# Kernel tuning notes

Measured on AMD Instinct MI355X. Metric: run time of the kernel, lower is better.

The kernel has to match this reference:

```python
import jax, jax.numpy as jnp
import numpy as np

# config constants (match init_kwargs)
C = 1024
NH = 16
HS = C // NH
CHUNK = 64          # attn_chunk_size
TOPK = 32           # attn_topk
WINDOW = 4096       # kv_cache_window_size
MIN_KV = 16384      # min_kv_cache_size
MAX_KV = 32768      # max_kv_cache_size
SHORT = 4096        # short_sequence_criteria
CT = 65536          # incoming kv-cache length


def setup_inputs() -> dict:
    key = jax.random.key(0)
    ks = jax.random.split(key, 7)
    s = 1.0 / np.sqrt(C)
    return {
        "x": jax.random.normal(ks[0], (C,), jnp.float32),
        "k_cache": jax.random.normal(ks[1], (1, CT, C), jnp.float32),
        "v_cache": jax.random.normal(ks[2], (1, CT, C), jnp.float32),
        "Wr": jax.random.normal(ks[3], (C, C), jnp.float32) * s,
        "Wk": jax.random.normal(ks[4], (C, C), jnp.float32) * s,
        "Wv": jax.random.normal(ks[5], (C, C), jnp.float32) * s,
        "Wo": jax.random.normal(ks[6], (C, C), jnp.float32) * s,
    }


def _split_heads(t):  # (1, T, C) -> (1, NH, T, HS)
    return t.reshape(1, t.shape[1], NH, HS).transpose(0, 2, 1, 3)


def _update_kv_cache(q, k_cache, v_cache):
    # q: (1,1,C); caches: (1,CT,C). CT > MIN_KV so compression runs.
    past = CT - WINDOW
    kp = _split_heads(k_cache[:, :past])          # (1,NH,past,HS)
    vp = _split_heads(v_cache[:, :past])
    qh = _split_heads(q)                          # (1,NH,1,HS)
    scores = jnp.einsum("bhqd,bhkd->bhqk", qh, kp) / np.sqrt(HS)
    w = jax.nn.softmax(scores, axis=-1)           # (1,NH,1,past)
    vote = w.sum(axis=-2)                         # (1,NH,past)
    keep = MIN_KV - WINDOW                        # per-head tokens kept
    _, idx = jax.lax.top_k(vote, keep)            # (1,NH,keep), descending vote order
    kpc = jnp.take_along_axis(kp, idx[..., None], axis=2)  # (1,NH,keep,HS)
    vpc = jnp.take_along_axis(vp, idx[..., None], axis=2)
    kpc = kpc.transpose(0, 2, 1, 3).reshape(1, keep, C)
    vpc = vpc.transpose(0, 2, 1, 3).reshape(1, keep, C)
    k_new = jnp.concatenate([kpc, k_cache[:, past:]], axis=1)  # (1, MIN_KV, C)
    v_new = jnp.concatenate([vpc, v_cache[:, past:]], axis=1)
    return k_new, v_new


def reference(x, k_cache, v_cache, Wr, Wk, Wv, Wo):
    x2 = x[None, None, :]                         # (1,1,C)
    q = x2 @ Wr.T
    k = x2 @ Wk.T
    v = x2 @ Wv.T

    # CT > MAX_KV -> compress cache (eviction via attention vote per head)
    k_cache, v_cache = _update_kv_cache(q, k_cache, v_cache)
    CT2 = k_cache.shape[1]                        # MIN_KV = 16384 > SHORT -> sparse path

    num_chunks = CT2 // CHUNK
    kc = k_cache.reshape(1, num_chunks, CHUNK, C)
    vc = v_cache.reshape(1, num_chunks, CHUNK, C)
    chunk_key = kc.mean(axis=2)                   # (1,num_chunks,C)
    chunk_score = jnp.einsum("bqc,bkc->bqk", q, chunk_key)
    _, tidx = jax.lax.top_k(chunk_score[0, 0], TOPK)  # (TOPK,)
    topk_k = kc[:, tidx].reshape(1, TOPK * CHUNK, C)
    topk_v = vc[:, tidx].reshape(1, TOPK * CHUNK, C)

    k_comb = jnp.concatenate([topk_k, k], axis=1)  # (1, TOPK*CHUNK+1, C)
    v_comb = jnp.concatenate([topk_v, v], axis=1)

    qh = _split_heads(q)                          # (1,NH,1,HS)
    kh = _split_heads(k_comb)
    vh = _split_heads(v_comb)
    attn = jax.nn.softmax(
        jnp.einsum("bhqd,bhkd->bhqk", qh, kh) / np.sqrt(HS), axis=-1)
    y = jnp.einsum("bhqk,bhkd->bhqd", attn, vh)   # (1,NH,1,HS)
    y = y.transpose(0, 2, 1, 3).reshape(C)
    y = y @ Wo.T
    return y
```

## Files before the change

### kernel.cpp

```cpp
#include <hip/hip_runtime.h>
#include <stdint.h>

#define C      1024
#define NH     16
#define HS     64
#define CT     65536
#define PAST   61440
#define KEEP   12288
#define NCOMP  192
#define NSEL   32
#define NB     8192
#define NBLK   256
#define FLAGW  8

typedef unsigned long long ull;

#define LD_A(p)   __hip_atomic_load((p), __ATOMIC_RELAXED, __HIP_MEMORY_SCOPE_AGENT)
#define ST_A(p,v) __hip_atomic_store((p), (v), __ATOMIC_RELAXED, __HIP_MEMORY_SCOPE_AGENT)

__device__ __forceinline__ unsigned int desc_key(float f) {
    unsigned int b = __float_as_uint(f);
    return (b >> 31) ? b : (~b & 0x7FFFFFFFu);
}
__device__ __forceinline__ float u_to_f(unsigned int u) {
    unsigned int b = (u & 0x80000000u) ? u : (0x7FFFFFFFu - u);
    return __uint_as_float(b);
}
__device__ __forceinline__ int bin_of(float s, float hi, float scale) {
    int b = (int)((hi - s) * scale);
    return b < 0 ? 0 : (b > NB - 1 ? NB - 1 : b);
}
__device__ __forceinline__ void load_params(const unsigned* umin, const unsigned* umax,
                                            int h, float* hi, float* sc) {
    float h2 = u_to_f(umin[h]);
    float lo = u_to_f(umax[h]);
    float r = h2 - lo;
    *hi = h2;
    *sc = (r > 0.f) ? (float)(NB - 1) / r : 0.f;
}

__device__ __forceinline__ void arrive(unsigned* flag, unsigned ph) {
    __syncthreads();
    if (threadIdx.x == 0) {
        asm volatile("s_waitcnt vmcnt(0)" ::: "memory");
        ST_A(&flag[blockIdx.x * FLAGW], ph);
    }
}
__device__ __forceinline__ void wait_head(unsigned* flag, unsigned ph, int h) {
    if (threadIdx.x < 16)
        while (LD_A(&flag[(h * 16 + threadIdx.x) * FLAGW]) < ph)
            __builtin_amdgcn_s_sleep(2);
    __syncthreads();
}
__device__ __forceinline__ void wait_all(unsigned* flag, unsigned ph) {
    if (threadIdx.x < 256)
        while (LD_A(&flag[threadIdx.x * FLAGW]) < ph)
            __builtin_amdgcn_s_sleep(2);
    __syncthreads();
}

__global__ void k_proj(const float* __restrict__ x, const float* __restrict__ Wr,
                       const float* __restrict__ Wk, const float* __restrict__ Wv,
                       float* __restrict__ q, float* __restrict__ kn, float* __restrict__ vn,
                       unsigned* __restrict__ hc, unsigned* __restrict__ umin,
                       unsigned* __restrict__ umax, ull* __restrict__ cs_fix,
                       unsigned* __restrict__ flag) {
    int gid = blockIdx.x * 256 + threadIdx.x;
    for (int i = gid; i < 2 * NH * NB; i += 196608) hc[i] = 0;
    if (blockIdx.x >= 512 && blockIdx.x < 520)
        flag[(blockIdx.x - 512) * 256 + threadIdx.x] = 0u;
    if (blockIdx.x == 700) {
        if (threadIdx.x < 16) umin[threadIdx.x] = 0xFFFFFFFFu;
        else if (threadIdx.x < 32) umax[threadIdx.x - 16] = 0u;
    }
    if (blockIdx.x == 701 && threadIdx.x < 256) cs_fix[threadIdx.x] = 0ull;

    int w = blockIdx.x * (blockDim.x >> 6) + (threadIdx.x >> 6);
    int lane = threadIdx.x & 63;
    int mat = w >> 10, row = w & 1023;
    const float* W = (mat == 0) ? Wr : (mat == 1) ? Wk : Wv;
    const float4* Wrow = (const float4*)(W + (size_t)row * C);
    const float4* x4 = (const float4*)x;
    float acc = 0.f;
#pragma unroll
    for (int i = 0; i < 4; ++i) {
        float4 a = Wrow[i * 64 + lane];
        float4 b = x4[i * 64 + lane];
        acc += a.x * b.x + a.y * b.y + a.z * b.z + a.w * b.w;
    }
#pragma unroll
    for (int off = 32; off; off >>= 1) acc += __shfl_xor(acc, off);
    if (lane == 0) { (mat == 0 ? q : (mat == 1 ? kn : vn))[row] = acc; }
}

__global__ __launch_bounds__(1024, 2) void k_mega(
        const float* __restrict__ kc, const float* __restrict__ vc,
        unsigned* __restrict__ umin, unsigned* __restrict__ umax,
        unsigned* __restrict__ hist, unsigned* __restrict__ cnt,
        ull* __restrict__ G, ull* __restrict__ stokv,
        ull* __restrict__ cs_fix, float* __restrict__ part,
        const float* __restrict__ q, const float* __restrict__ kn,
        const float* __restrict__ vn, const float* __restrict__ Wo,
        float* __restrict__ yg, float* __restrict__ out,
        float* __restrict__ s_win, unsigned* __restrict__ flag) {
    const int bid = blockIdx.x, tid = threadIdx.x;
    const int lane = tid & 63, wave = tid >> 6;
    const int h = bid >> 4, seg = bid & 15;
    __shared__ __align__(16) char smem[50688];
    __shared__ unsigned shT, shN;
    __shared__ unsigned wsum[16];
    __shared__ float smn[16], smx[16];

    float* s_lds = (float*)smem;
    unsigned* lh = (unsigned*)(smem + 16384);

    {
        const int t_base = seg * 4096;
        const int g = lane >> 4;
        float4 qv = ((const float4*)q)[h * 16 + (lane & 15)];
        float mn = 3.4e38f, mx = -3.4e38f;
        for (int ib = 0; ib < 64; ib += 4) {
            float4 av[4];
#pragma unroll
            for (int u = 0; u < 4; ++u) {
                int lt = wave * 256 + (ib + u) * 4 + g;
                av[u] = ((const float4*)(kc + (size_t)(t_base + lt) * C + h * HS))[lane & 15];
            }
#pragma unroll
            for (int u = 0; u < 4; ++u) {
                float d = av[u].x * qv.x + av[u].y * qv.y + av[u].z * qv.z + av[u].w * qv.w;
#pragma unroll
                for (int off = 8; off; off >>= 1) d += __shfl_xor(d, off);
                int lt = wave * 256 + (ib + u) * 4 + g;
                if ((lane & 15) == 0) s_lds[lt] = d;
                mn = fminf(mn, d);
                mx = fmaxf(mx, d);
            }
        }
        __syncthreads();
        if (seg < 15) {
#pragma unroll
            for (int off = 32; off; off >>= 1) {
                mn = fminf(mn, __shfl_xor(mn, off));
                mx = fmaxf(mx, __shfl_xor(mx, off));
            }
            if (lane == 0) { smn[wave] = mn; smx[wave] = mx; }
            __syncthreads();
            if (tid == 0) {
                float bmn = smn[0], bmx = smx[0];
                for (int w2 = 1; w2 < 16; ++w2) {
                    bmn = fminf(bmn, smn[w2]);
                    bmx = fmaxf(bmx, smx[w2]);
                }
                atomicMin(&umin[h], desc_key(bmx));
                atomicMax(&umax[h], desc_key(bmn));
            }
        } else {
            for (int i = tid; i < 4096; i += 1024)
                ST_A(&s_win[h * 4096 + i], s_lds[i]);
            int c = tid >> 4;
            long long f = 0;
#pragma unroll
            for (int j = 0; j < 4; ++j)
                f += llrintf(s_lds[c * 64 + (tid & 15) * 4 + j] * 16777216.f);
#pragma unroll
            for (int off = 8; off; off >>= 1) f += __shfl_xor(f, off);
            if ((tid & 15) == 0) atomicAdd(&cs_fix[NCOMP + c], (ull)f);
        }
    }
    arrive(flag, 1); wait_head(flag, 1, h);

    float hi, sc; load_params(umin, umax, h, &hi, &sc);

    {
        for (int i = tid; i < NB; i += 1024) lh[i] = 0;
        __syncthreads();
        if (seg < 15) {
            for (int i = tid; i < 4096; i += 1024)
                atomicAdd(&lh[bin_of(s_lds[i], hi, sc)], 1u);
            __syncthreads();
            unsigned* gh = hist + h * NB;
            for (int i = tid; i < NB; i += 1024) {
                unsigned c = lh[i];
                if (c) atomicAdd(&gh[i], c);
            }
        }
    }
    arrive(flag, 2); wait_head(flag, 2, h);

    {
        const unsigned* gh = hist + h * NB;
        unsigned c8[8]; unsigned loc = 0; int b0 = tid * 8;
#pragma unroll
        for (int k = 0; k < 8; ++k) { c8[k] = gh[b0 + k]; loc += c8[k]; }
        unsigned run = loc;
#pragma unroll
        for (int off = 1; off < 64; off <<= 1) {
            unsigned n = __shfl_up(run, off);
            if (lane >= off) run += n;
        }
        if (lane == 63) wsum[wave] = run;
        __syncthreads();
        if (wave == 0 && lane < 16) {
            unsigned v = wsum[lane];
#pragma unroll
            for (int off = 1; off < 16; off <<= 1) {
                unsigned n = __shfl_up(v, off);
                if (lane >= off) v += n;
            }
            wsum[lane] = v;
        }
        __syncthreads();
        unsigned r = run - loc + (wave ? wsum[wave - 1] : 0u);
#pragma unroll
        for (int k = 0; k < 8; ++k) {
            unsigned c = c8[k];
            lh[b0 + k] = r;
            unsigned inc = r + c;
            if (r < KEEP && inc >= KEEP) { shT = (unsigned)(b0 + k); shN = inc; }
            r = inc;
        }
    }
    __syncthreads();
    const unsigned T = shT, ncand = shN;

    if (seg < 15) {
        unsigned* ch = cnt + h * NB;
        ull* Gh = G + (size_t)h * 65536;
        const int t_base = seg * 4096;
        for (int i = tid; i < 4096; i += 1024) {
            float v = s_lds[i];
            int b = bin_of(v, hi, sc);
            if ((unsigned)b <= T) {
                unsigned pos = lh[b] + atomicAdd(&ch[b], 1u);
                ST_A(&Gh[pos], ((ull)desc_key(v) << 16) | (unsigned)(t_base + i));
            }
        }
    }
    arrive(flag, 3); wait_head(flag, 3, h);

    {
        ull* csl = (ull*)(smem + 49152);
        if (tid < NCOMP) csl[tid] = 0ull;
        __syncthreads();
        const ull* Gh = G + (size_t)h * 65536;
        for (unsigned p = seg * 1024 + tid; p < ncand; p += 16384) {
            ull pk = Gh[p];
            unsigned u = (unsigned)(pk >> 16);
            float v = u_to_f(u);
            int b = bin_of(v, hi, sc);
            unsigned start = lh[b];
            unsigned end = (b == NB - 1) ? ncand : lh[b + 1];
            unsigned rank = start;
            for (unsigned j = start; j < end; ++j) rank += (Gh[j] < pk) ? 1u : 0u;
            if (rank < KEEP) {
                ST_A(&stokv[h * KEEP + rank], pk);
                long long f = llrintf(v * 16777216.f);
                atomicAdd(&csl[rank >> 6], (ull)f);
            }
        }
        __syncthreads();
        if (tid < NCOMP) {
            ull c = csl[tid];
            if (c) atomicAdd(&cs_fix[tid], c);
        }
    }
    arrive(flag, 4); wait_all(flag, 4);

    {
        ull* key = (ull*)smem;
        unsigned* sel_l = (unsigned*)(smem + 2048);
        float* scm = (float*)(smem + 2176);
        float* exb = (float*)(smem + 2688);
        float* vbuf = (float*)(smem + 3200);
        if (tid < 256) {
            long long v = (long long)cs_fix[tid];
            ull bb = (ull)(v + (1ll << 45));
            key[tid] = (((1ull << 46) - bb) << 8) | (unsigned)tid;
        }
        __syncthreads();
        for (unsigned k = 2; k <= 256; k <<= 1) {
            for (unsigned j = k >> 1; j > 0; j >>= 1) {
                if (tid < 256) {
                    unsigned ixj = tid ^ j;
                    if (ixj > (unsigned)tid) {
                        ull a = key[tid], b = key[ixj];
                        bool up = ((tid & k) == 0);
                        if (up ? (a > b) : (a < b)) { key[tid] = b; key[ixj] = a; }
                    }
                }
                __syncthreads();
            }
        }
        if (tid < NSEL) sel_l[tid] = (unsigned)(key[tid] & 0xFFull);
        __syncthreads();

        int su = tid >> 9, sid = tid & 511;
        int p = bid * 2 + su;
        int hh = p >> 5, ci = p & 31;
        int c = (int)sel_l[ci];
        int g = sid >> 3, q8 = sid & 7;
        int t; float sv;
        if (c < NCOMP) {
            ull pk = stokv[hh * KEEP + c * 64 + g];
            t = (int)(pk & 0xFFFFull);
            sv = u_to_f((unsigned)(pk >> 16));
        } else {
            int j = (c - NCOMP) * 64 + g;
            t = PAST + j;
            sv = s_win[hh * 4096 + j];
        }
        if (q8 == 0) scm[su * 64 + g] = sv * 0.125f;
        __syncthreads();
        float m = -1e30f;
        for (int j = 0; j < 64; ++j) m = fmaxf(m, scm[su * 64 + j]);
        float e = expf(scm[su * 64 + g] - m);
        if (q8 == 0) exb[su * 64 + g] = e;
        const float4* vrow = (const float4*)(vc + (size_t)t * C + hh * HS);
        float4 v0 = vrow[q8 * 2], v1 = vrow[q8 * 2 + 1];
        float* vb = vbuf + su * 4352 + g * 68 + q8 * 8;
        vb[0] = e * v0.x; vb[1] = e * v0.y; vb[2] = e * v0.z; vb[3] = e * v0.w;
        vb[4] = e * v1.x; vb[5] = e * v1.y; vb[6] = e * v1.z; vb[7] = e * v1.w;
        __syncthreads();
        if (sid < 64) {
            float acc = 0.f;
            for (int g2 = 0; g2 < 64; ++g2) acc += vbuf[su * 4352 + g2 * 68 + sid];
            float* P = part + (size_t)(hh * 32 + ci) * 68;
            ST_A(&P[2 + sid], acc);
            if (sid == 0) {
                float es = 0.f;
                for (int g2 = 0; g2 < 64; ++g2) es += exb[su * 64 + g2];
                ST_A(&P[0], m);
                ST_A(&P[1], es);
            }
        }
    }
    arrive(flag, 5); wait_head(flag, 5, h);

    int row = bid * 4 + (wave >> 2), qtr = wave & 3;
    const float4* Wrow4 = (const float4*)(Wo + (size_t)row * C) + qtr * 64;
    float4 wa = Wrow4[lane];

    if (seg == 0 && tid < 64) {
        float p = q[h * 64 + tid] * kn[h * 64 + tid];
#pragma unroll
        for (int off = 32; off; off >>= 1) p += __shfl_xor(p, off);
        float a_new = p * 0.125f;
        const float* P0 = part + (size_t)h * 32 * 68;
        float m = a_new;
        for (int ci = 0; ci < 32; ++ci) m = fmaxf(m, P0[ci * 68]);
        float den = expf(a_new - m);
        float acc = den * vn[h * HS + tid];
        for (int ci = 0; ci < 32; ++ci) {
            float w = expf(P0[ci * 68] - m);
            den += w * P0[ci * 68 + 1];
            acc += w * P0[ci * 68 + 2 + tid];
        }
        ST_A(&yg[h * HS + tid], acc / den);
    }
    if (seg == 0) arrive(flag, 6);
    if (tid < 16)
        while (LD_A(&flag[(tid * 16) * FLAGW]) < 6u) __builtin_amdgcn_s_sleep(2);
    __syncthreads();

    {
        float* yl = (float*)smem;
        float* ps = (float*)(smem + 4096);
        yl[tid] = yg[tid];
        __syncthreads();
        const float4* y4 = (const float4*)yl + qtr * 64;
        float4 b = y4[lane];
        float acc = wa.x * b.x + wa.y * b.y + wa.z * b.z + wa.w * b.w;
#pragma unroll
        for (int off = 32; off; off >>= 1) acc += __shfl_xor(acc, off);
        if (lane == 0) ps[wave] = acc;
        __syncthreads();
        if (tid < 4)
            out[bid * 4 + tid] = ps[tid * 4] + ps[tid * 4 + 1] + ps[tid * 4 + 2] + ps[tid * 4 + 3];
    }
}

extern "C" void kernel_launch(void* const* d_in, const int* in_sizes, int n_in,
                              void* d_out, int out_size, void* d_ws, size_t ws_size,
                              hipStream_t stream) {
    const float* x  = (const float*)d_in[0];
    const float* kc = (const float*)d_in[1];
    const float* vc = (const float*)d_in[2];
    const float* Wr = (const float*)d_in[3];
    const float* Wk = (const float*)d_in[4];
    const float* Wv = (const float*)d_in[5];
    const float* Wo = (const float*)d_in[6];
    float* out = (float*)d_out;
    char* ws = (char*)d_ws;

    float* q    = (float*)(ws + 0);
    float* kn   = (float*)(ws + 8192);
    float* vn   = (float*)(ws + 16384);
    ull* cs_fix = (ull*)(ws + 32768);
    float* yg   = (float*)(ws + 40960);
    float* part = (float*)(ws + 49152);
    unsigned* umin = (unsigned*)(ws + 188416);
    unsigned* umax = (unsigned*)(ws + 188480);
    unsigned* flag = (unsigned*)(ws + 192512);
    float* s_win   = (float*)(ws + 262144);
    ull* stokv     = (ull*)(ws + 524288);
    unsigned* hist = (unsigned*)(ws + 2097152);
    unsigned* cnt  = (unsigned*)(ws + 2621440);
    ull* G = (ull*)(ws + 3145728);

    k_proj<<<768, 256, 0, stream>>>(x, Wr, Wk, Wv, q, kn, vn, hist, umin, umax, cs_fix, flag);
    k_mega<<<NBLK, 1024, 0, stream>>>(kc, vc, umin, umax, hist, cnt, G, stokv, cs_fix,
                                      part, q, kn, vn, Wo, yg, out, s_win, flag);
}
```

Before: 115.5 us.

## Double persistent block count to 512, halving per-block token segment

```diff
diff --git a/kernel.cpp b/kernel.cpp
--- a/kernel.cpp
+++ b/kernel.cpp
@@ -10,7 +10,7 @@
 #define NCOMP  192
 #define NSEL   32
 #define NB     8192
-#define NBLK   256
+#define NBLK   512
 #define FLAGW  8
 
 typedef unsigned long long ull;
@@ -47,13 +47,13 @@
     }
 }
 __device__ __forceinline__ void wait_head(unsigned* flag, unsigned ph, int h) {
-    if (threadIdx.x < 16)
-        while (LD_A(&flag[(h * 16 + threadIdx.x) * FLAGW]) < ph)
+    if (threadIdx.x < 32)
+        while (LD_A(&flag[(h * 32 + threadIdx.x) * FLAGW]) < ph)
             __builtin_amdgcn_s_sleep(2);
     __syncthreads();
 }
 __device__ __forceinline__ void wait_all(unsigned* flag, unsigned ph) {
-    if (threadIdx.x < 256)
+    if (threadIdx.x < NBLK)
         while (LD_A(&flag[threadIdx.x * FLAGW]) < ph)
             __builtin_amdgcn_s_sleep(2);
     __syncthreads();
@@ -67,7 +67,7 @@
                        unsigned* __restrict__ flag) {
     int gid = blockIdx.x * 256 + threadIdx.x;
     for (int i = gid; i < 2 * NH * NB; i += 196608) hc[i] = 0;
-    if (blockIdx.x >= 512 && blockIdx.x < 520)
+    if (blockIdx.x >= 512 && blockIdx.x < 528)
         flag[(blockIdx.x - 512) * 256 + threadIdx.x] = 0u;
     if (blockIdx.x == 700) {
         if (threadIdx.x < 16) umin[threadIdx.x] = 0xFFFFFFFFu;
@@ -93,7 +93,7 @@
     if (lane == 0) { (mat == 0 ? q : (mat == 1 ? kn : vn))[row] = acc; }
 }
 
-__global__ __launch_bounds__(1024, 2) void k_mega(
+__global__ __launch_bounds__(1024, 8) void k_mega(
         const float* __restrict__ kc, const float* __restrict__ vc,
         unsigned* __restrict__ umin, unsigned* __restrict__ umax,
         unsigned* __restrict__ hist, unsigned* __restrict__ cnt,
@@ -105,25 +105,25 @@
         float* __restrict__ s_win, unsigned* __restrict__ flag) {
     const int bid = blockIdx.x, tid = threadIdx.x;
     const int lane = tid & 63, wave = tid >> 6;
-    const int h = bid >> 4, seg = bid & 15;
-    __shared__ __align__(16) char smem[50688];
+    const int h = bid >> 5, seg = bid & 31;
+    __shared__ __align__(16) char smem[43008];
     __shared__ unsigned shT, shN;
     __shared__ unsigned wsum[16];
     __shared__ float smn[16], smx[16];
 
     float* s_lds = (float*)smem;
-    unsigned* lh = (unsigned*)(smem + 16384);
-
-    {
-        const int t_base = seg * 4096;
+    unsigned* lh = (unsigned*)(smem + 8192);
+
+    {
+        const int t_base = seg * 2048;
         const int g = lane >> 4;
         float4 qv = ((const float4*)q)[h * 16 + (lane & 15)];
         float mn = 3.4e38f, mx = -3.4e38f;
-        for (int ib = 0; ib < 64; ib += 4) {
+        for (int ib = 0; ib < 32; ib += 4) {
             float4 av[4];
 #pragma unroll
             for (int u = 0; u < 4; ++u) {
-                int lt = wave * 256 + (ib + u) * 4 + g;
+                int lt = wave * 128 + (ib + u) * 4 + g;
                 av[u] = ((const float4*)(kc + (size_t)(t_base + lt) * C + h * HS))[lane & 15];
             }
 #pragma unroll
@@ -131,14 +131,14 @@
                 float d = av[u].x * qv.x + av[u].y * qv.y + av[u].z * qv.z + av[u].w * qv.w;
 #pragma unroll
                 for (int off = 8; off; off >>= 1) d += __shfl_xor(d, off);
-                int lt = wave * 256 + (ib + u) * 4 + g;
+                int lt = wave * 128 + (ib + u) * 4 + g;
                 if ((lane & 15) == 0) s_lds[lt] = d;
                 mn = fminf(mn, d);
                 mx = fmaxf(mx, d);
             }
         }
         __syncthreads();
-        if (seg < 15) {
+        if (seg < 30) {
 #pragma unroll
             for (int off = 32; off; off >>= 1) {
                 mn = fminf(mn, __shfl_xor(mn, off));
@@ -156,16 +156,19 @@
                 atomicMax(&umax[h], desc_key(bmn));
             }
         } else {
-            for (int i = tid; i < 4096; i += 1024)
-                ST_A(&s_win[h * 4096 + i], s_lds[i]);
-            int c = tid >> 4;
-            long long f = 0;
-#pragma unroll
-            for (int j = 0; j < 4; ++j)
-                f += llrintf(s_lds[c * 64 + (tid & 15) * 4 + j] * 16777216.f);
-#pragma unroll
-            for (int off = 8; off; off >>= 1) f += __shfl_xor(f, off);
-            if ((tid & 15) == 0) atomicAdd(&cs_fix[NCOMP + c], (ull)f);
+            for (int i = tid; i < 2048; i += 1024)
+                ST_A(&s_win[h * 4096 + (seg - 30) * 2048 + i], s_lds[i]);
+            if (tid < 512) {
+                int c = tid >> 4;
+                long long f = 0;
+#pragma unroll
+                for (int j = 0; j < 4; ++j)
+                    f += llrintf(s_lds[c * 64 + (tid & 15) * 4 + j] * 16777216.f);
+#pragma unroll
+                for (int off = 8; off; off >>= 1) f += __shfl_xor(f, off);
+                if ((tid & 15) == 0)
+                    atomicAdd(&cs_fix[NCOMP + (seg - 30) * 32 + c], (ull)f);
+            }
         }
     }
     arrive(flag, 1); wait_head(flag, 1, h);
@@ -175,8 +178,8 @@
     {
         for (int i = tid; i < NB; i += 1024) lh[i] = 0;
         __syncthreads();
-        if (seg < 15) {
-            for (int i = tid; i < 4096; i += 1024)
+        if (seg < 30) {
+            for (int i = tid; i < 2048; i += 1024)
                 atomicAdd(&lh[bin_of(s_lds[i], hi, sc)], 1u);
             __syncthreads();
             unsigned* gh = hist + h * NB;
@@ -224,11 +227,11 @@
     __syncthreads();
     const unsigned T = shT, ncand = shN;
 
-    if (seg < 15) {
+    if (seg < 30) {
         unsigned* ch = cnt + h * NB;
         ull* Gh = G + (size_t)h * 65536;
-        const int t_base = seg * 4096;
-        for (int i = tid; i < 4096; i += 1024) {
+        const int t_base = seg * 2048;
+        for (int i = tid; i < 2048; i += 1024) {
             float v = s_lds[i];
             int b = bin_of(v, hi, sc);
             if ((unsigned)b <= T) {
@@ -240,11 +243,11 @@
     arrive(flag, 3); wait_head(flag, 3, h);
 
     {
-        ull* csl = (ull*)(smem + 49152);
+        ull* csl = (ull*)(smem + 40960);
         if (tid < NCOMP) csl[tid] = 0ull;
         __syncthreads();
         const ull* Gh = G + (size_t)h * 65536;
-        for (unsigned p = seg * 1024 + tid; p < ncand; p += 16384) {
+        for (unsigned p = seg * 1024 + tid; p < ncand; p += 32768) {
             ull pk = Gh[p];
             unsigned u = (unsigned)(pk >> 16);
             float v = u_to_f(u);
@@ -271,8 +274,8 @@
         ull* key = (ull*)smem;
         unsigned* sel_l = (unsigned*)(smem + 2048);
         float* scm = (float*)(smem + 2176);
-        float* exb = (float*)(smem + 2688);
-        float* vbuf = (float*)(smem + 3200);
+        float* exb = (float*)(smem + 2432);
+        float* vbuf = (float*)(smem + 2688);
         if (tid < 256) {
             long long v = (long long)cs_fix[tid];
             ull bb = (ull)(v + (1ll << 45));
@@ -295,11 +298,9 @@
         if (tid < NSEL) sel_l[tid] = (unsigned)(key[tid] & 0xFFull);
         __syncthreads();
 
-        int su = tid >> 9, sid = tid & 511;
-        int p = bid * 2 + su;
-        int hh = p >> 5, ci = p & 31;
+        int hh = h, ci = seg;
         int c = (int)sel_l[ci];
-        int g = sid >> 3, q8 = sid & 7;
+        int g = tid >> 4, q16 = tid & 15;
         int t; float sv;
         if (c < NCOMP) {
             ull pk = stokv[hh * KEEP + c * 64 + g];
@@ -310,26 +311,24 @@
             t = PAST + j;
             sv = s_win[hh * 4096 + j];
         }
-        if (q8 == 0) scm[su * 64 + g] = sv * 0.125f;
+        if (q16 == 0) scm[g] = sv * 0.125f;
         __syncthreads();
         float m = -1e30f;
-        for (int j = 0; j < 64; ++j) m = fmaxf(m, scm[su * 64 + j]);
-        float e = expf(scm[su * 64 + g] - m);
-        if (q8 == 0) exb[su * 64 + g] = e;
-        const float4* vrow = (const float4*)(vc + (size_t)t * C + hh * HS);
-        float4 v0 = vrow[q8 * 2], v1 = vrow[q8 * 2 + 1];
-        float* vb = vbuf + su * 4352 + g * 68 + q8 * 8;
+        for (int j = 0; j < 64; ++j) m = fmaxf(m, scm[j]);
+        float e = expf(scm[g] - m);
+        if (q16 == 0) exb[g] = e;
+        float4 v0 = ((const float4*)(vc + (size_t)t * C + hh * HS))[q16];
+        float* vb = vbuf + g * 68 + q16 * 4;
         vb[0] = e * v0.x; vb[1] = e * v0.y; vb[2] = e * v0.z; vb[3] = e * v0.w;
-        vb[4] = e * v1.x; vb[5] = e * v1.y; vb[6] = e * v1.z; vb[7] = e * v1.w;
-        __syncthreads();
-        if (sid < 64) {
+        __syncthreads();
+        if (tid < 64) {
             float acc = 0.f;
-            for (int g2 = 0; g2 < 64; ++g2) acc += vbuf[su * 4352 + g2 * 68 + sid];
+            for (int g2 = 0; g2 < 64; ++g2) acc += vbuf[g2 * 68 + tid];
             float* P = part + (size_t)(hh * 32 + ci) * 68;
-            ST_A(&P[2 + sid], acc);
-            if (sid == 0) {
+            ST_A(&P[2 + tid], acc);
+            if (tid == 0) {
                 float es = 0.f;
-                for (int g2 = 0; g2 < 64; ++g2) es += exb[su * 64 + g2];
+                for (int g2 = 0; g2 < 64; ++g2) es += exb[g2];
                 ST_A(&P[0], m);
                 ST_A(&P[1], es);
             }
@@ -337,9 +336,9 @@
     }
     arrive(flag, 5); wait_head(flag, 5, h);
 
-    int row = bid * 4 + (wave >> 2), qtr = wave & 3;
-    const float4* Wrow4 = (const float4*)(Wo + (size_t)row * C) + qtr * 64;
-    float4 wa = Wrow4[lane];
+    int row = bid * 2 + (wave >> 2), qtr = wave & 3;
+    float4 wa = make_float4(0.f, 0.f, 0.f, 0.f);
+    if (wave < 8) wa = ((const float4*)(Wo + (size_t)row * C))[qtr * 64 + lane];
 
     if (seg == 0 && tid < 64) {
         float p = q[h * 64 + tid] * kn[h * 64 + tid];
@@ -360,7 +359,7 @@
     }
     if (seg == 0) arrive(flag, 6);
     if (tid < 16)
-        while (LD_A(&flag[(tid * 16) * FLAGW]) < 6u) __builtin_amdgcn_s_sleep(2);
+        while (LD_A(&flag[(tid * 32) * FLAGW]) < 6u) __builtin_amdgcn_s_sleep(2);
     __syncthreads();
 
     {
@@ -368,15 +367,17 @@
         float* ps = (float*)(smem + 4096);
         yl[tid] = yg[tid];
         __syncthreads();
-        const float4* y4 = (const float4*)yl + qtr * 64;
-        float4 b = y4[lane];
-        float acc = wa.x * b.x + wa.y * b.y + wa.z * b.z + wa.w * b.w;
-#pragma unroll
-        for (int off = 32; off; off >>= 1) acc += __shfl_xor(acc, off);
-        if (lane == 0) ps[wave] = acc;
-        __syncthreads();
-        if (tid < 4)
-            out[bid * 4 + tid] = ps[tid * 4] + ps[tid * 4 + 1] + ps[tid * 4 + 2] + ps[tid * 4 + 3];
+        if (wave < 8) {
+            const float4* y4 = (const float4*)yl + qtr * 64;
+            float4 b = y4[lane];
+            float acc = wa.x * b.x + wa.y * b.y + wa.z * b.z + wa.w * b.w;
+#pragma unroll
+            for (int off = 32; off; off >>= 1) acc += __shfl_xor(acc, off);
+            if (lane == 0) ps[wave] = acc;
+        }
+        __syncthreads();
+        if (tid < 2)
+            out[bid * 2 + tid] = ps[tid * 4] + ps[tid * 4 + 1] + ps[tid * 4 + 2] + ps[tid * 4 + 3];
     }
 }
 
```

Result: slower. 154.0 us (+33.3%).
